# Kernel optimization log

Hardware: AMD Instinct MI355X
Metric: run time of the kernel (lower is better)

## Reference

```python
import jax, jax.numpy as jnp
import numpy as np

B, T, S, A = 4, 10, 6, 6
HID, L, IMG = 512, 6, 128
NCH = 16  # spatial-softmax channels
_px, _py = np.meshgrid(np.linspace(-1.0, 1.0, IMG), np.linspace(-1.0, 1.0, IMG))
POSX = jnp.asarray(_px.reshape(-1), jnp.float32)
POSY = jnp.asarray(_py.reshape(-1), jnp.float32)


def _conv_relu(x, w, b):
    y = jax.lax.conv_general_dilated(x, w, (1, 1), 'SAME',
                                     dimension_numbers=('NCHW', 'OIHW', 'NCHW'))
    return jax.nn.relu(y + b[None, :, None, None])


def _cnn_ss(x, ws, bs):
    for w, b in zip(ws, bs):
        x = _conv_relu(x, w, b)
    n = x.shape[0]
    attn = jax.nn.softmax(x.reshape(n, NCH, -1), axis=-1)  # (n, 16, H*W)
    ex = attn @ POSX  # (n, 16)
    ey = attn @ POSY
    return jnp.stack([ex, ey], axis=-1).reshape(n, 2 * NCH)  # (n, 32)


def _lstm_cell(x, h, c, wih, whh, bih, bhh):
    g = x @ wih.T + bih + h @ whh.T + bhh
    i, f, gg, o = jnp.split(g, 4, axis=-1)  # torch LSTMCell gate order i,f,g,o
    c2 = jax.nn.sigmoid(f) * c + jax.nn.sigmoid(i) * jnp.tanh(gg)
    h2 = jax.nn.sigmoid(o) * jnp.tanh(c2)
    return h2, c2


def setup_inputs() -> dict:
    key = jax.random.key(0)
    ks = iter(jax.random.split(key, 64))

    def nrm(shape, s=0.05):
        return jax.random.normal(next(ks), shape, dtype=jnp.float32) * s

    inp = {
        'seq_img_main': nrm((B, T, 3, IMG, IMG), 1.0),
        'seq_img_secondary': nrm((B, T, 3, IMG, IMG), 1.0),
        'seq_states': nrm((B, T, S), 1.0),
    }
    chans = [(32, 3), (64, 32), (128, 64), (16, 128)]
    for cam in ('m', 's'):
        for j, (o, ci) in enumerate(chans):
            inp[f'{cam}_w{j}'] = nrm((o, ci, 3, 3))
            inp[f'{cam}_b{j}'] = nrm((o,))
    in0, inr = S + 64, HID + 64  # 70 and 576
    inp['wih0'] = nrm((4 * HID, in0)); inp['whh0'] = nrm((4 * HID, HID))
    inp['bih0'] = nrm((4 * HID,)); inp['bhh0'] = nrm((4 * HID,))
    inp['wih_r'] = nrm((L - 1, 4 * HID, inr)); inp['whh_r'] = nrm((L - 1, 4 * HID, HID))
    inp['bih_r'] = nrm((L - 1, 4 * HID)); inp['bhh_r'] = nrm((L - 1, 4 * HID))
    inp['out_w'] = nrm((A, inr)); inp['out_b'] = nrm((A,))
    return inp


def reference(seq_img_main, seq_img_secondary, seq_states,
              m_w0, m_b0, m_w1, m_b1, m_w2, m_b2, m_w3, m_b3,
              s_w0, s_b0, s_w1, s_b1, s_w2, s_b2, s_w3, s_b3,
              wih0, whh0, bih0, bhh0, wih_r, whh_r, bih_r, bhh_r,
              out_w, out_b):
    b, t = seq_img_main.shape[:2]
    fm = _cnn_ss(seq_img_main.reshape(b * t, 3, IMG, IMG),
                 [m_w0, m_w1, m_w2, m_w3], [m_b0, m_b1, m_b2, m_b3])
    fs = _cnn_ss(seq_img_secondary.reshape(b * t, 3, IMG, IMG),
                 [s_w0, s_w1, s_w2, s_w3], [s_b0, s_b1, s_b2, s_b3])
    img = jnp.concatenate([fm, fs], axis=-1).reshape(b, t, 64)  # (B,T,64)

    h0 = jnp.zeros((L, b, HID), jnp.float32)
    c0 = jnp.zeros((L, b, HID), jnp.float32)

    def step(carry, xt):
        h, c = carry
        st, im = xt  # (B,S), (B,64)
        x = jnp.concatenate([st, im], axis=-1)
        hn, cn = _lstm_cell(x, h[0], c[0], wih0, whh0, bih0, bhh0)
        hs, cs = [hn], [cn]
        for l in range(L - 1):
            x = jnp.concatenate([hs[-1], im], axis=-1)
            hl, cl = _lstm_cell(x, h[l + 1], c[l + 1],
                                wih_r[l], whh_r[l], bih_r[l], bhh_r[l])
            hs.append(hl); cs.append(cl)
        out = jnp.concatenate([hs[-1], im], axis=-1) @ out_w.T + out_b
        return (jnp.stack(hs), jnp.stack(cs)), out

    _, outs = jax.lax.scan(step, (h0, c0),
                           (seq_states.transpose(1, 0, 2), img.transpose(1, 0, 2)))
    return outs.transpose(1, 0, 2)  # (B,T,A)
```

## Files before the change

kernel.cpp:

```cpp
#include <hip/hip_runtime.h>
#include <hip/hip_bf16.h>
#include <math.h>

typedef __hip_bfloat16 bf16;
typedef short bf16x8 __attribute__((ext_vector_type(8)));
typedef float f32x4 __attribute__((ext_vector_type(4)));

static constexpr int HWPX = 16384;
static constexpr int NBL  = 16;

__device__ inline float sigmoidf_(float x) { return 1.0f / (1.0f + expf(-x)); }
__device__ inline float bflo(unsigned u) { return __uint_as_float(u << 16); }
__device__ inline float bfhi(unsigned u) { return __uint_as_float(u & 0xffff0000u); }
__device__ inline int swz(int x) { return (x ^ (x >> 2)) & 3; }

__device__ inline void gll16(const bf16* g, short* l) {
    __builtin_amdgcn_global_load_lds(
        (const __attribute__((address_space(1))) void*)g,
        (__attribute__((address_space(3))) void*)l, 16, 0, 0);
}

__global__ __launch_bounds__(256) void prep_lstm_k(
    const float* __restrict__ wih0, const float* __restrict__ whh0,
    const float* __restrict__ wihr, const float* __restrict__ whhr,
    bf16* __restrict__ d0, bf16* __restrict__ d1,
    bf16* __restrict__ d2, bf16* __restrict__ d3)
{
    const size_t nA = 2048ull * 72, nB = 2048ull * 512;
    const size_t nC = 5ull * 2048 * 576, nD = 5ull * 2048 * 512;
    for (size_t i = blockIdx.x * 256ull + threadIdx.x; i < nA + nB + nC + nD;
         i += (size_t)gridDim.x * 256) {
        if (i < nA) {
            int c = (int)(i % 72), r = (int)(i / 72);
            d0[i] = __float2bfloat16(c < 70 ? wih0[(size_t)r * 70 + c] : 0.f);
        } else if (i < nA + nB) {
            size_t k = i - nA; d1[k] = __float2bfloat16(whh0[k]);
        } else if (i < nA + nB + nC) {
            size_t k = i - nA - nB; d2[k] = __float2bfloat16(wihr[k]);
        } else {
            size_t k = i - nA - nB - nC; d3[k] = __float2bfloat16(whhr[k]);
        }
    }
}

struct ConvW {
    const float* src[8];
    bf16* dst[8];
};

__global__ __launch_bounds__(256) void prep_conv_k(ConvW a)
{
    const int sizes[4] = {3072, 18432, 73728, 18432};
    const int cins[4] = {3, 32, 64, 128};
    const int couts[4] = {32, 64, 128, 16};
    int total = 2 * 113664;
    for (int idx = blockIdx.x * 256 + threadIdx.x; idx < total; idx += gridDim.x * 256) {
        int i = idx, cam = 0;
        if (i >= 113664) { cam = 1; i -= 113664; }
        int layer = 0;
        while (layer < 3 && i >= sizes[layer]) { i -= sizes[layer]; ++layer; }
        const float* w = a.src[cam * 4 + layer];
        bf16* d = a.dst[cam * 4 + layer];
        if (layer == 0) {
            int k = i & 31, co = (i >> 5) & 31, ky = i >> 10;
            int kx = k >> 3, c = k & 7;
            float v = (kx < 3 && c < 3) ? w[((co * 3 + c) * 3 + ky) * 3 + kx] : 0.f;
            d[i] = __float2bfloat16(v);
        } else {
            int CIN = cins[layer], COUT = couts[layer], KC = CIN / 32;
            int e = i & 7;
            int t2 = i >> 3;
            int co = t2 % COUT;
            int t3 = t2 / COUT;
            int q = t3 & 3;
            int t4 = t3 >> 2;
            int kc = t4 % KC;
            int tap = t4 / KC;
            d[i] = __float2bfloat16(w[((size_t)(co * CIN + kc * 32 + q * 8 + e)) * 9 + tap]);
        }
    }
}

__global__ __launch_bounds__(256) void conv0_nhwc(
    const float* __restrict__ srcm, const float* __restrict__ srcs,
    const bf16* __restrict__ w0m, const bf16* __restrict__ w0s,
    const float* __restrict__ bm, const float* __restrict__ bs,
    bf16* __restrict__ out, int c0)
{
    const int y = blockIdx.x;
    const int cam = blockIdx.y;
    const int img = blockIdx.z;
    const int ci_ = cam * gridDim.z + img;
    const float* inImg = (cam ? srcs : srcm) + (size_t)(c0 + img) * 3 * HWPX;
    const bf16* wT0 = cam ? w0s : w0m;
    const float* bias = cam ? bs : bm;
    const int tid = threadIdx.x;
    const int wave = tid >> 6, lane = tid & 63;
    const int wm = wave & 1, wn = wave >> 1;
    const int q = lane >> 4, n16 = lane & 15;

    __shared__ short smem[3 * 130 * 16];

    for (int d = tid; d < 3 * 130; d += 256) {
        int x = d % 130, r = d / 130;
        int yy = y + r - 1, xx = x - 1;
        bf16 v8[8];
#pragma unroll
        for (int c = 0; c < 8; ++c) v8[c] = __float2bfloat16(0.f);
        if ((unsigned)yy < 128u && (unsigned)xx < 128u) {
            int o = yy * 128 + xx;
            v8[0] = __float2bfloat16(inImg[o]);
            v8[1] = __float2bfloat16(inImg[HWPX + o]);
            v8[2] = __float2bfloat16(inImg[2 * HWPX + o]);
        }
        *(bf16x8*)(void*)&smem[(r * 130 + x) * 16] = *(bf16x8*)(void*)v8;
        *(bf16x8*)(void*)&smem[(r * 130 + x) * 16 + 8] = (bf16x8)0;
    }
    __syncthreads();

    f32x4 acc[4];
#pragma unroll
    for (int nt = 0; nt < 4; ++nt) acc[nt] = f32x4{0.f, 0.f, 0.f, 0.f};

    const int co = wm * 16 + n16;
#pragma unroll
    for (int ky = 0; ky < 3; ++ky) {
        bf16x8 aF = *(const bf16x8*)(const void*)(wT0 + ((size_t)(ky * 32 + co) * 32) + q * 8);
#pragma unroll
        for (int nt = 0; nt < 4; ++nt) {
            int x = (wn * 4 + nt) * 16 + n16;
            int off = (q < 3) ? (ky * 130 + x + q) * 16 : (ky * 130 + x) * 16 + 8;
            bf16x8 bF = *(const bf16x8*)(const void*)&smem[off];
            acc[nt] = __builtin_amdgcn_mfma_f32_16x16x32_bf16(aF, bF, acc[nt], 0, 0, 0);
        }
    }

    int co0 = wm * 16 + q * 4;
#pragma unroll
    for (int nt = 0; nt < 4; ++nt) {
        int x = (wn * 4 + nt) * 16 + n16;
        bf16 tmp[4];
#pragma unroll
        for (int r = 0; r < 4; ++r) {
            float v = acc[nt][r] + bias[co0 + r];
            tmp[r] = __float2bfloat16(v > 0.f ? v : 0.f);
        }
        *reinterpret_cast<uint2*>(out + ((size_t)ci_ * HWPX + y * 128 + x) * 32 + co0)
            = *reinterpret_cast<uint2*>(tmp);
    }
}

template <int CIN, int COUT>
__global__ __launch_bounds__(256, 4) void conv2r(
    const bf16* __restrict__ in, const bf16* __restrict__ wTm,
    const bf16* __restrict__ wTs, const float* __restrict__ bm,
    const float* __restrict__ bs, bf16* __restrict__ out,
    const char* __restrict__ zpage)
{
    constexpr int KC = CIN / 32;
    constexpr int NB = (KC > 1) ? 2 : 1;
    constexpr int MW = COUT / 32;
    constexpr int SLOTS = 4 * 264;

    const int y0 = (blockIdx.x >> 1) * 2;
    const int x0 = (blockIdx.x & 1) * 64;
    const int cam = blockIdx.y;
    const int img = blockIdx.z;
    const int ci_ = cam * gridDim.z + img;
    const bf16* wT = cam ? wTs : wTm;
    const float* bias = cam ? bs : bm;
    const int tid = threadIdx.x;
    const int wave = tid >> 6, lane = tid & 63;
    const int wrow = wave >> 1, wm = wave & 1;
    const int q = lane >> 4, n16 = lane & 15;

    __shared__ short smem[NB][SLOTS * 8];
    const bf16* inImg = in + (size_t)ci_ * HWPX * CIN;

    const bf16* sptr[5];
#pragma unroll
    for (int it = 0; it < 5; ++it) {
        int s = it * 256 + tid;
        int r = s / 264, s2 = s - r * 264;
        int sx = s2 >> 2;
        int g = (s2 & 3) ^ swz(sx);
        int yy = y0 + r - 1, xx = x0 + sx - 1;
        bool ok = (s < SLOTS) && ((unsigned)yy < 128u) && ((unsigned)xx < 128u);
        sptr[it] = ok ? inImg + ((size_t)yy * 128 + xx) * CIN + g * 8
                      : (const bf16*)(zpage + (tid & 255) * 16);
    }
    auto stage = [&](int kc, int buf) {
#pragma unroll
        for (int it = 0; it < 5; ++it) {
            if (it * 256 + tid < SLOTS)
                gll16(sptr[it] + kc * 32, &smem[buf][it * 2048 + wave * 512]);
        }
    };

    f32x4 acc[MW][4];
#pragma unroll
    for (int mt = 0; mt < MW; ++mt)
#pragma unroll
        for (int nt = 0; nt < 4; ++nt) acc[mt][nt] = f32x4{0.f, 0.f, 0.f, 0.f};

    stage(0, 0);
    for (int kc = 0; kc < KC; ++kc) {
        __syncthreads();
        if (kc + 1 < KC) stage(kc + 1, (kc + 1) % NB);
        const short* sb = smem[kc % NB];
#pragma unroll
        for (int ky = 0; ky < 3; ++ky) {
#pragma unroll
            for (int kx = 0; kx < 3; ++kx) {
                bf16x8 aF[MW];
#pragma unroll
                for (int mt = 0; mt < MW; ++mt) {
                    int co = (wm * MW + mt) * 16 + n16;
                    aF[mt] = *(const bf16x8*)(const void*)(wT +
                        ((((size_t)(ky * 3 + kx) * KC + kc) * 4 + q) * COUT + co) * 8);
                }
#pragma unroll
                for (int nt = 0; nt < 4; ++nt) {
                    int xt = nt * 16 + n16 + kx;
                    int slot = (wrow + ky) * 264 + xt * 4 + (q ^ swz(xt));
                    bf16x8 bF = *(const bf16x8*)(const void*)&sb[slot * 8];
#pragma unroll
                    for (int mt = 0; mt < MW; ++mt)
                        acc[mt][nt] = __builtin_amdgcn_mfma_f32_16x16x32_bf16(
                            aF[mt], bF, acc[mt][nt], 0, 0, 0);
                }
            }
        }
    }

    const int y = y0 + wrow;
#pragma unroll
    for (int mt = 0; mt < MW; ++mt) {
        int co0 = (wm * MW + mt) * 16 + q * 4;
#pragma unroll
        for (int nt = 0; nt < 4; ++nt) {
            int x = x0 + nt * 16 + n16;
            bf16 tmp[4];
#pragma unroll
            for (int r = 0; r < 4; ++r) {
                float v = acc[mt][nt][r] + bias[co0 + r];
                tmp[r] = __float2bfloat16(v > 0.f ? v : 0.f);
            }
            *reinterpret_cast<uint2*>(out + ((size_t)ci_ * HWPX + y * 128 + x) * COUT + co0)
                = *reinterpret_cast<uint2*>(tmp);
        }
    }
}

__global__ __launch_bounds__(256, 6) void conv4_xs(
    const bf16* __restrict__ in, const bf16* __restrict__ wTm,
    const bf16* __restrict__ wTs, const float* __restrict__ bm,
    const float* __restrict__ bs,
    float* __restrict__ partial,
    const char* __restrict__ zpage, int c0)
{
    constexpr int CIN = 128, COUT = 16, KC = 4;
    constexpr int SLOTS = 3 * 66 * 4;
    const int y = blockIdx.x >> 1;
    const int xh = blockIdx.x & 1;
    const int x0 = xh * 64;
    const int cam = blockIdx.y;
    const int img = blockIdx.z;
    const int ci_ = cam * gridDim.z + img;
    const int gimg = cam * 40 + c0 + img;
    const bf16* wT = cam ? wTs : wTm;
    const float* bias = cam ? bs : bm;
    const int tid = threadIdx.x;
    const int wave = tid >> 6, lane = tid & 63;
    const int q = lane >> 4, n16 = lane & 15;

    __shared__ short smem[2][SLOTS * 8];
    __shared__ float sred[3][4][16];
    const bf16* inImg = in + (size_t)ci_ * HWPX * CIN;

    const bf16* sptr[4];
#pragma unroll
    for (int it = 0; it < 4; ++it) {
        int s = it * 256 + tid;
        int r = s / 264, s2 = s - r * 264;
        int sx = s2 >> 2;
        int g = (s2 & 3) ^ swz(sx);
        int yy = y + r - 1, xx = x0 + sx - 1;
        bool ok = (s < SLOTS) && ((unsigned)yy < 128u) && ((unsigned)xx < 128u);
        sptr[it] = ok ? inImg + ((size_t)yy * 128 + xx) * CIN + g * 8
                      : (const bf16*)(zpage + (tid & 255) * 16);
    }
    auto stage = [&](int kc, int buf) {
#pragma unroll
        for (int it = 0; it < 4; ++it) {
            if (it * 256 + tid < SLOTS)
                gll16(sptr[it] + kc * 32, &smem[buf][it * 2048 + wave * 512]);
        }
    };

    f32x4 acc = f32x4{0.f, 0.f, 0.f, 0.f};

    stage(0, 0);
    for (int kc = 0; kc < KC; ++kc) {
        __syncthreads();
        if (kc + 1 < KC) stage(kc + 1, (kc + 1) & 1);
        const short* sb = smem[kc & 1];
#pragma unroll
        for (int ky = 0; ky < 3; ++ky) {
#pragma unroll
            for (int kx = 0; kx < 3; ++kx) {
                bf16x8 aF = *(const bf16x8*)(const void*)(wT +
                    ((((size_t)(ky * 3 + kx) * KC + kc) * 4 + q) * COUT + n16) * 8);
                int xt = wave * 16 + n16 + kx;
                int slot = xt * 4 + (q ^ swz(xt));
                bf16x8 bF = *(const bf16x8*)(const void*)&sb[ky * 2112 + slot * 8];
                acc = __builtin_amdgcn_mfma_f32_16x16x32_bf16(aF, bF, acc, 0, 0, 0);
            }
        }
    }

    float v[4];
    int x = x0 + wave * 16 + n16;
    float px = -1.f + (2.f / 127.f) * x;
#pragma unroll
    for (int r = 0; r < 4; ++r) {
        float t = acc[r] + bias[q * 4 + r];
        v[r] = t > 0.f ? t : 0.f;
    }
    float M[4];
#pragma unroll
    for (int r = 0; r < 4; ++r) {
        M[r] = v[r];
        M[r] = fmaxf(M[r], __shfl_xor(M[r], 1));
        M[r] = fmaxf(M[r], __shfl_xor(M[r], 2));
        M[r] = fmaxf(M[r], __shfl_xor(M[r], 4));
        M[r] = fmaxf(M[r], __shfl_xor(M[r], 8));
    }
    if (n16 == 0)
#pragma unroll
        for (int r = 0; r < 4; ++r) sred[0][wave][q * 4 + r] = M[r];
    __syncthreads();
#pragma unroll
    for (int r = 0; r < 4; ++r) {
        M[r] = fmaxf(fmaxf(sred[0][0][q * 4 + r], sred[0][1][q * 4 + r]),
                     fmaxf(sred[0][2][q * 4 + r], sred[0][3][q * 4 + r]));
    }
    float s[4], sx[4];
#pragma unroll
    for (int r = 0; r < 4; ++r) {
        float e = expf(v[r] - M[r]);
        s[r] = e; sx[r] = e * px;
        s[r] += __shfl_xor(s[r], 1);  sx[r] += __shfl_xor(sx[r], 1);
        s[r] += __shfl_xor(s[r], 2);  sx[r] += __shfl_xor(sx[r], 2);
        s[r] += __shfl_xor(s[r], 4);  sx[r] += __shfl_xor(sx[r], 4);
        s[r] += __shfl_xor(s[r], 8);  sx[r] += __shfl_xor(sx[r], 8);
    }
    __syncthreads();
    if (n16 == 0)
#pragma unroll
        for (int r = 0; r < 4; ++r) {
            sred[1][wave][q * 4 + r] = s[r];
            sred[2][wave][q * 4 + r] = sx[r];
        }
    __syncthreads();
    if (tid < 16) {
        float S = sred[1][0][tid] + sred[1][1][tid] + sred[1][2][tid] + sred[1][3][tid];
        float SX = sred[2][0][tid] + sred[2][1][tid] + sred[2][2][tid] + sred[2][3][tid];
        float Mv = fmaxf(fmaxf(sred[0][0][tid], sred[0][1][tid]),
                         fmaxf(sred[0][2][tid], sred[0][3][tid]));
        float* pp = partial + (((size_t)gimg * 16 + tid) * 256 + (y * 2 + xh)) * 4;
        pp[0] = Mv; pp[1] = S; pp[2] = SX;
    }
}

__global__ __launch_bounds__(256) void ssmerge_k(
    const float* __restrict__ partial, float* __restrict__ featm,
    float* __restrict__ feats)
{
    const int img = blockIdx.x;
    const int cam = img / 40, li = img % 40;
    float* feat = cam ? feats : featm;
    const int tid = threadIdx.x;
    const int co = tid >> 4, s = tid & 15;
    const float* base = partial + ((size_t)img * 16 + co) * 256 * 4;
    float M = -1e30f, S = 0.f, SX = 0.f, SY = 0.f;
    for (int i = s; i < 256; i += 16) {
        float m = base[i * 4], sv = base[i * 4 + 1], sxv = base[i * 4 + 2];
        float py = -1.f + (2.f / 127.f) * (i >> 1);
        float Mn = fmaxf(M, m);
        float w0 = expf(M - Mn), w1 = expf(m - Mn);
        S = S * w0 + sv * w1;
        SX = SX * w0 + sxv * w1;
        SY = SY * w0 + sv * py * w1;
        M = Mn;
    }
#pragma unroll
    for (int mask = 1; mask < 16; mask <<= 1) {
        float Mo = __shfl_xor(M, mask), So = __shfl_xor(S, mask);
        float SXo = __shfl_xor(SX, mask), SYo = __shfl_xor(SY, mask);
        float Mn = fmaxf(M, Mo);
        float w0 = expf(M - Mn), w1 = expf(Mo - Mn);
        S = S * w0 + So * w1; SX = SX * w0 + SXo * w1; SY = SY * w0 + SYo * w1;
        M = Mn;
    }
    if (s == 0) {
        feat[(size_t)li * 32 + 2 * co] = SX / S;
        feat[(size_t)li * 32 + 2 * co + 1] = SY / S;
    }
}

__device__ inline float imgfeat(const float* featm, const float* feats,
                                int b, int t, int k)
{
    int idx = (b * 10 + t) * 32;
    return k < 32 ? featm[idx + k] : feats[idx + k - 32];
}

template <int NB1>
__device__ inline void cell_mm(const bf16* __restrict__ wih,
                               const bf16* __restrict__ whh,
                               const float* __restrict__ xs0,
                               int j, int sub, float (&dg)[4][4])
{
    constexpr int K1 = NB1 * 8;
    constexpr int XS = K1 + 512;
#pragma unroll
    for (int r = 0; r < 4; ++r) {
        const uint4* __restrict__ w1 =
            reinterpret_cast<const uint4*>(wih + (size_t)(j + r * 512) * K1);
#pragma unroll
        for (int g0 = 0; g0 < NB1; g0 += 8) {
            int g = g0 + sub;
            if (g0 + 7 < NB1 || g < NB1) {
                uint4 u = w1[g];
                float a0 = bflo(u.x), a1 = bfhi(u.x), a2 = bflo(u.y), a3 = bfhi(u.y);
                float a4 = bflo(u.z), a5 = bfhi(u.z), a6 = bflo(u.w), a7 = bfhi(u.w);
#pragma unroll
                for (int b = 0; b < 4; ++b) {
                    const float* xp = xs0 + b * XS + g * 8;
                    dg[r][b] += a0 * xp[0] + a1 * xp[1] + a2 * xp[2] + a3 * xp[3]
                              + a4 * xp[4] + a5 * xp[5] + a6 * xp[6] + a7 * xp[7];
                }
            }
        }
        const uint4* __restrict__ w2 =
            reinterpret_cast<const uint4*>(whh + (size_t)(j + r * 512) * 512);
#pragma unroll
        for (int gi = 0; gi < 8; ++gi) {
            int g = gi * 8 + sub;
            uint4 u = w2[g];
            float a0 = bflo(u.x), a1 = bfhi(u.x), a2 = bflo(u.y), a3 = bfhi(u.y);
            float a4 = bflo(u.z), a5 = bfhi(u.z), a6 = bflo(u.w), a7 = bfhi(u.w);
#pragma unroll
            for (int b = 0; b < 4; ++b) {
                const float* xp = xs0 + b * XS + K1 + g * 8;
                dg[r][b] += a0 * xp[0] + a1 * xp[1] + a2 * xp[2] + a3 * xp[3]
                          + a4 * xp[4] + a5 * xp[5] + a6 * xp[6] + a7 * xp[7];
            }
        }
    }
}

template <int NB1>
__device__ inline void cell_step(
    int l, int t, int bx,
    const bf16* __restrict__ wih, const bf16* __restrict__ whh,
    const float* __restrict__ bih, const float* __restrict__ bhh,
    const float* __restrict__ states,
    const float* __restrict__ featm, const float* __restrict__ feats,
    float* __restrict__ hAll, float* __restrict__ cst,
    float* __restrict__ xs)
{
    constexpr int K1 = NB1 * 8;
    constexpr int XS = K1 + 512;
    const int tid = threadIdx.x;
    const int jloc = tid >> 3;
    const int sub = tid & 7;
    const int j = bx * 32 + jloc;

    const float* hprev = (l == 0) ? nullptr
                       : hAll + ((size_t)(t + 1) * 6 + (l - 1)) * 2048;
    const float* hold  = hAll + ((size_t)t * 6 + l) * 2048;
    float* hnew        = hAll + ((size_t)(t + 1) * 6 + l) * 2048;

    if (NB1 == 72) {
        for (int i = tid; i < 4 * 512; i += 256) {
            int bb = i >> 9, kk = i & 511;
            float2 cv;
            int base;
            if (kk < 256) {
                cv = *reinterpret_cast<const float2*>(&hprev[bb * 512 + kk * 2]);
                base = bb * XS + kk * 2;
            } else {
                cv = *reinterpret_cast<const float2*>(&hold[bb * 512 + (kk - 256) * 2]);
                base = bb * XS + 576 + (kk - 256) * 2;
            }
            xs[base] = cv.x; xs[base + 1] = cv.y;
        }
        {
            int bb = tid >> 6, k = tid & 63;
            xs[bb * XS + 512 + k] = imgfeat(featm, feats, bb, t, k);
        }
    } else {
        for (int i = tid; i < 4 * 256; i += 256) {
            int bb = i >> 8, kk = i & 255;
            float2 cv = *reinterpret_cast<const float2*>(&hold[bb * 512 + kk * 2]);
            int base = bb * XS + 72 + kk * 2;
            xs[base] = cv.x; xs[base + 1] = cv.y;
        }
        for (int i = tid; i < 4 * 72; i += 256) {
            int bb = i / 72, k = i - bb * 72;
            float v = (k < 6) ? states[(bb * 10 + t) * 6 + k]
                              : (k < 70 ? imgfeat(featm, feats, bb, t, k - 6) : 0.f);
            xs[bb * XS + k] = v;
        }
    }
    __syncthreads();

    float dg[4][4] = {{0.f, 0.f, 0.f, 0.f}, {0.f, 0.f, 0.f, 0.f},
                      {0.f, 0.f, 0.f, 0.f}, {0.f, 0.f, 0.f, 0.f}};
    cell_mm<NB1>(wih, whh, xs, j, sub, dg);

#pragma unroll
    for (int r = 0; r < 4; ++r)
#pragma unroll
        for (int b = 0; b < 4; ++b) {
            dg[r][b] += __shfl_xor(dg[r][b], 1);
            dg[r][b] += __shfl_xor(dg[r][b], 2);
            dg[r][b] += __shfl_xor(dg[r][b], 4);
        }

    if (sub == 0) {
        float b0 = bih[j] + bhh[j];
        float b1 = bih[j + 512] + bhh[j + 512];
        float b2 = bih[j + 1024] + bhh[j + 1024];
        float b3 = bih[j + 1536] + bhh[j + 1536];
#pragma unroll
        for (int b = 0; b < 4; ++b) {
            float gi = dg[0][b] + b0;
            float gf = dg[1][b] + b1;
            float gg = dg[2][b] + b2;
            float go = dg[3][b] + b3;
            float cp = cst[b * 512 + j];
            float c2 = sigmoidf_(gf) * cp + sigmoidf_(gi) * tanhf(gg);
            float h2 = sigmoidf_(go) * tanhf(c2);
            cst[b * 512 + j] = c2;
            hnew[b * 512 + j] = h2;
        }
    }
}

__global__ __launch_bounds__(256) void lstm_diag2_k(
    const bf16* __restrict__ wih0p, const bf16* __restrict__ whh0b,
    const bf16* __restrict__ wihrb, const bf16* __restrict__ whhrb,
    const float* __restrict__ bih0, const float* __restrict__ bhh0,
    const float* __restrict__ bihr, const float* __restrict__ bhhr,
    const float* __restrict__ states,
    const float* __restrict__ featm, const float* __restrict__ feats,
    float* __restrict__ hAll, float* __restrict__ cAll,
    const float* __restrict__ out_w, const float* __restrict__ out_b,
    float* __restrict__ out, int d)
{
    const int l = blockIdx.y;
    const int bx = blockIdx.x;
    const int tid = threadIdx.x;
    __shared__ float xs[4 * 1088];

    if (l == 6) {
        int t = d - 6;
        if (t < 0 || t >= 10 || bx != 0) return;
        const float* h5 = hAll + ((size_t)(t + 1) * 6 + 5) * 2048;
        int p = tid >> 3, sub = tid & 7;
        if (p >= 24) return;
        int b = p / 6, a = p % 6;
        const float* wr = out_w + a * 576;
        float acc = 0.f;
        for (int k = sub; k < 256; k += 8) {
            float2 cv = *reinterpret_cast<const float2*>(&h5[b * 512 + k * 2]);
            acc += wr[k * 2] * cv.x + wr[k * 2 + 1] * cv.y;
        }
        for (int k = sub; k < 64; k += 8)
            acc += wr[512 + k] * imgfeat(featm, feats, b, t, k);
        acc += __shfl_xor(acc, 1);
        acc += __shfl_xor(acc, 2);
        acc += __shfl_xor(acc, 4);
        if (sub == 0) out[(b * 10 + t) * 6 + a] = acc + out_b[a];
        return;
    }

    const int t = d - l;
    if (t < 0 || t >= 10) return;

    float* cst = cAll + (size_t)l * 2048;
    if (l == 0) {
        cell_step<9>(0, t, bx, wih0p, whh0b, bih0, bhh0,
                     states, featm, feats, hAll, cst, xs);
    } else {
        const bf16* wih = wihrb + (size_t)(l - 1) * 2048 * 576;
        const bf16* whh = whhrb + (size_t)(l - 1) * 2048 * 512;
        const float* bih = bihr + (l - 1) * 2048;
        const float* bhh = bhhr + (l - 1) * 2048;
        cell_step<72>(l, t, bx, wih, whh, bih, bhh,
                      states, featm, feats, hAll, cst, xs);
    }
}

extern "C" void kernel_launch(void* const* d_in, const int* in_sizes, int n_in,
                              void* d_out, int out_size, void* d_ws, size_t ws_size,
                              hipStream_t stream)
{
    const float* seq_m = (const float*)d_in[0];
    const float* seq_s = (const float*)d_in[1];
    const float* states = (const float*)d_in[2];
    const float *cw[2][4], *cb[2][4];
    for (int cam = 0; cam < 2; ++cam)
        for (int j = 0; j < 4; ++j) {
            cw[cam][j] = (const float*)d_in[3 + cam * 8 + j * 2];
            cb[cam][j] = (const float*)d_in[3 + cam * 8 + j * 2 + 1];
        }
    const float* wih0  = (const float*)d_in[19];
    const float* whh0  = (const float*)d_in[20];
    const float* bih0  = (const float*)d_in[21];
    const float* bhh0  = (const float*)d_in[22];
    const float* wih_r = (const float*)d_in[23];
    const float* whh_r = (const float*)d_in[24];
    const float* bih_r = (const float*)d_in[25];
    const float* bhh_r = (const float*)d_in[26];
    const float* out_w = (const float*)d_in[27];
    const float* out_b = (const float*)d_in[28];
    float* out = (float*)d_out;

    char* wsc = (char*)d_ws;
    auto carve = [&](size_t bytes) {
        char* p = wsc;
        wsc += (bytes + 255) & ~(size_t)255;
        return p;
    };
    float* featm = (float*)carve(40 * 32 * 4);
    float* feats = (float*)carve(40 * 32 * 4);
    float* hAll  = (float*)carve((size_t)11 * 6 * 2048 * 4);
    float* cAll  = (float*)carve((size_t)6 * 2048 * 4);
    char*  zpage = carve(8192);
    float* partial = (float*)carve((size_t)80 * 16 * 256 * 4 * 4);
    const int wtElts[4] = {3072, 18432, 73728, 18432};
    bf16* wT[2][4];
    for (int cam = 0; cam < 2; ++cam)
        for (int j = 0; j < 4; ++j) wT[cam][j] = (bf16*)carve(wtElts[j] * 2);
    bf16* wih0p = (bf16*)carve((size_t)2048 * 72 * 2);
    bf16* whh0b = (bf16*)carve((size_t)2048 * 512 * 2);
    bf16* wihrb = (bf16*)carve((size_t)5 * 2048 * 576 * 2);
    bf16* whhrb = (bf16*)carve((size_t)5 * 2048 * 512 * 2);

    size_t used = (size_t)(wsc - (char*)d_ws);
    size_t rem = ws_size > used ? ws_size - used : 0;
    int CHI = 1;
    const int cands[7] = {20, 10, 8, 5, 4, 2, 1};
    for (int i = 0; i < 7; ++i) {
        size_t need = (size_t)2 * cands[i] * (128 + 64) * HWPX * 2;
        if (need <= rem) { CHI = cands[i]; break; }
    }
    bf16* bufA = (bf16*)carve((size_t)2 * CHI * HWPX * 128 * 2);
    bf16* bufB = (bf16*)carve((size_t)2 * CHI * HWPX * 64 * 2);

    hipMemsetAsync(hAll, 0, 6 * 2048 * 4, stream);
    hipMemsetAsync(cAll, 0, 6 * 2048 * 4, stream);
    hipMemsetAsync(zpage, 0, 8192, stream);

    prep_lstm_k<<<2048, 256, 0, stream>>>(wih0, whh0, wih_r, whh_r,
                                          wih0p, whh0b, wihrb, whhrb);
    ConvW cwArg;
    for (int cam = 0; cam < 2; ++cam)
        for (int j = 0; j < 4; ++j) {
            cwArg.src[cam * 4 + j] = cw[cam][j];
            cwArg.dst[cam * 4 + j] = wT[cam][j];
        }
    prep_conv_k<<<888, 256, 0, stream>>>(cwArg);

    for (int c0 = 0; c0 < 40; c0 += CHI) {
        int ch = (40 - c0) < CHI ? (40 - c0) : CHI;
        conv0_nhwc<<<dim3(128, 2, ch), 256, 0, stream>>>(
            seq_m, seq_s, wT[0][0], wT[1][0], cb[0][0], cb[1][0], bufA, c0);
        conv2r<32, 64><<<dim3(128, 2, ch), 256, 0, stream>>>(
            bufA, wT[0][1], wT[1][1], cb[0][1], cb[1][1], bufB, zpage);
        conv2r<64, 128><<<dim3(128, 2, ch), 256, 0, stream>>>(
            bufB, wT[0][2], wT[1][2], cb[0][2], cb[1][2], bufA, zpage);
        conv4_xs<<<dim3(256, 2, ch), 256, 0, stream>>>(
            bufA, wT[0][3], wT[1][3], cb[0][3], cb[1][3], partial, zpage, c0);
    }
    ssmerge_k<<<80, 256, 0, stream>>>(partial, featm, feats);

    for (int d = 0; d < 16; ++d) {
        lstm_diag2_k<<<dim3(16, 7), 256, 0, stream>>>(
            wih0p, whh0b, wihrb, whhrb, bih0, bhh0, bih_r, bhh_r,
            states, featm, feats, hAll, cAll, out_w, out_b, out, d);
    }
}
```

Measured before the change: 1.149 ms.

## Fuse first two conv layers into one kernel with halo recompute in LDS

Merges conv0 (3->32) and conv1 (32->64) into a single kernel. Each block recomputes the conv0 output for a 2-row by 64-column tile plus a halo and stores it in swizzled LDS, then runs conv1 straight from LDS. This removes the global write and read of the 32-channel intermediate and one kernel launch, at the cost of redundant halo compute and more LDS per block. It also adds a chunk-size candidate of 40 images so that all images can be processed in one pass when the workspace allows.

```diff
diff --git a/kernel.cpp b/kernel.cpp
--- a/kernel.cpp
+++ b/kernel.cpp
@@ -7,7 +7,6 @@
 typedef float f32x4 __attribute__((ext_vector_type(4)));
 
 static constexpr int HWPX = 16384;
-static constexpr int NBL  = 16;
 
 __device__ inline float sigmoidf_(float x) { return 1.0f / (1.0f + expf(-x)); }
 __device__ inline float bflo(unsigned u) { return __uint_as_float(u << 16); }
@@ -81,29 +80,41 @@
     }
 }
 
-__global__ __launch_bounds__(256) void conv0_nhwc(
+__global__ __launch_bounds__(256, 4) void conv01(
     const float* __restrict__ srcm, const float* __restrict__ srcs,
     const bf16* __restrict__ w0m, const bf16* __restrict__ w0s,
+    const float* __restrict__ b0m, const float* __restrict__ b0s,
+    const bf16* __restrict__ wTm, const bf16* __restrict__ wTs,
     const float* __restrict__ bm, const float* __restrict__ bs,
     bf16* __restrict__ out, int c0)
 {
-    const int y = blockIdx.x;
+    constexpr int COUT = 64, MW = 2;
+    constexpr int SLOTS = 4 * 264;
+
+    const int y0 = (blockIdx.x >> 1) * 2;
+    const int x0 = (blockIdx.x & 1) * 64;
     const int cam = blockIdx.y;
     const int img = blockIdx.z;
     const int ci_ = cam * gridDim.z + img;
     const float* inImg = (cam ? srcs : srcm) + (size_t)(c0 + img) * 3 * HWPX;
     const bf16* wT0 = cam ? w0s : w0m;
+    const float* bias0 = cam ? b0s : b0m;
+    const bf16* wT = cam ? wTs : wTm;
     const float* bias = cam ? bs : bm;
     const int tid = threadIdx.x;
     const int wave = tid >> 6, lane = tid & 63;
-    const int wm = wave & 1, wn = wave >> 1;
+    const int wrow = wave >> 1, wm = wave & 1;
     const int q = lane >> 4, n16 = lane & 15;
 
-    __shared__ short smem[3 * 130 * 16];
-
-    for (int d = tid; d < 3 * 130; d += 256) {
-        int x = d % 130, r = d / 130;
-        int yy = y + r - 1, xx = x - 1;
+    __shared__ short smem[SLOTS * 8];
+    __shared__ short raw[6 * 68 * 16];
+
+    for (int i = tid; i < SLOTS; i += 256)
+        *(bf16x8*)(void*)&smem[i * 8] = (bf16x8)0;
+
+    for (int d = tid; d < 6 * 68; d += 256) {
+        int x = d % 68, r = d / 68;
+        int yy = y0 - 2 + r, xx = x0 - 2 + x;
         bf16 v8[8];
 #pragma unroll
         for (int c = 0; c < 8; ++c) v8[c] = __float2bfloat16(0.f);
@@ -113,40 +124,91 @@
             v8[1] = __float2bfloat16(inImg[HWPX + o]);
             v8[2] = __float2bfloat16(inImg[2 * HWPX + o]);
         }
-        *(bf16x8*)(void*)&smem[(r * 130 + x) * 16] = *(bf16x8*)(void*)v8;
-        *(bf16x8*)(void*)&smem[(r * 130 + x) * 16 + 8] = (bf16x8)0;
+        *(bf16x8*)(void*)&raw[d * 16] = *(bf16x8*)(void*)v8;
+        *(bf16x8*)(void*)&raw[d * 16 + 8] = (bf16x8)0;
     }
     __syncthreads();
 
-    f32x4 acc[4];
-#pragma unroll
-    for (int nt = 0; nt < 4; ++nt) acc[nt] = f32x4{0.f, 0.f, 0.f, 0.f};
-
-    const int co = wm * 16 + n16;
+    const int co0_ = wm * 16 + n16;
+    for (int rp = 0; rp < 4; ++rp) {
+        int Y = y0 - 1 + rp;
+        if ((unsigned)Y >= 128u) continue;
+        for (int xg = wrow; xg < 5; xg += 2) {
+            int xt = xg * 16 + n16;
+            int xts = xt < 66 ? xt : 65;
+            f32x4 a0 = f32x4{0.f, 0.f, 0.f, 0.f};
+#pragma unroll
+            for (int ky = 0; ky < 3; ++ky) {
+                bf16x8 aF = *(const bf16x8*)(const void*)(wT0 +
+                    ((size_t)(ky * 32 + co0_) * 32) + q * 8);
+                int off = (q < 3) ? ((rp + ky) * 68 + xts + q) * 16
+                                  : ((rp + ky) * 68 + xts) * 16 + 8;
+                bf16x8 bF = *(const bf16x8*)(const void*)&raw[off];
+                a0 = __builtin_amdgcn_mfma_f32_16x16x32_bf16(aF, bF, a0, 0, 0, 0);
+            }
+            int X = x0 - 1 + xt;
+            if (xt < 66 && (unsigned)X < 128u) {
+                int cb0 = wm * 16 + q * 4;
+                bf16 tmp[4];
+#pragma unroll
+                for (int r = 0; r < 4; ++r) {
+                    float v = a0[r] + bias0[cb0 + r];
+                    tmp[r] = __float2bfloat16(v > 0.f ? v : 0.f);
+                }
+                int g = cb0 >> 3;
+                int sbase = (rp * 264 + xt * 4 + (g ^ swz(xt))) * 8 + (q & 1) * 4;
+                *reinterpret_cast<uint2*>(&smem[sbase]) = *reinterpret_cast<uint2*>(tmp);
+            }
+        }
+    }
+    __syncthreads();
+
+    f32x4 acc[MW][4];
+#pragma unroll
+    for (int mt = 0; mt < MW; ++mt)
+#pragma unroll
+        for (int nt = 0; nt < 4; ++nt) acc[mt][nt] = f32x4{0.f, 0.f, 0.f, 0.f};
+
 #pragma unroll
     for (int ky = 0; ky < 3; ++ky) {
-        bf16x8 aF = *(const bf16x8*)(const void*)(wT0 + ((size_t)(ky * 32 + co) * 32) + q * 8);
+#pragma unroll
+        for (int kx = 0; kx < 3; ++kx) {
+            bf16x8 aF[MW];
+#pragma unroll
+            for (int mt = 0; mt < MW; ++mt) {
+                int co = (wm * MW + mt) * 16 + n16;
+                aF[mt] = *(const bf16x8*)(const void*)(wT +
+                    (((size_t)(ky * 3 + kx) * 4 + q) * COUT + co) * 8);
+            }
+#pragma unroll
+            for (int nt = 0; nt < 4; ++nt) {
+                int xt = nt * 16 + n16 + kx;
+                int slot = (wrow + ky) * 264 + xt * 4 + (q ^ swz(xt));
+                bf16x8 bF = *(const bf16x8*)(const void*)&smem[slot * 8];
+#pragma unroll
+                for (int mt = 0; mt < MW; ++mt)
+                    acc[mt][nt] = __builtin_amdgcn_mfma_f32_16x16x32_bf16(
+                        aF[mt], bF, acc[mt][nt], 0, 0, 0);
+            }
+        }
+    }
+
+    const int y = y0 + wrow;
+#pragma unroll
+    for (int mt = 0; mt < MW; ++mt) {
+        int co0 = (wm * MW + mt) * 16 + q * 4;
 #pragma unroll
         for (int nt = 0; nt < 4; ++nt) {
-            int x = (wn * 4 + nt) * 16 + n16;
-            int off = (q < 3) ? (ky * 130 + x + q) * 16 : (ky * 130 + x) * 16 + 8;
-            bf16x8 bF = *(const bf16x8*)(const void*)&smem[off];
-            acc[nt] = __builtin_amdgcn_mfma_f32_16x16x32_bf16(aF, bF, acc[nt], 0, 0, 0);
-        }
-    }
-
-    int co0 = wm * 16 + q * 4;
-#pragma unroll
-    for (int nt = 0; nt < 4; ++nt) {
-        int x = (wn * 4 + nt) * 16 + n16;
-        bf16 tmp[4];
-#pragma unroll
-        for (int r = 0; r < 4; ++r) {
-            float v = acc[nt][r] + bias[co0 + r];
-            tmp[r] = __float2bfloat16(v > 0.f ? v : 0.f);
-        }
-        *reinterpret_cast<uint2*>(out + ((size_t)ci_ * HWPX + y * 128 + x) * 32 + co0)
-            = *reinterpret_cast<uint2*>(tmp);
+            int x = x0 + nt * 16 + n16;
+            bf16 tmp[4];
+#pragma unroll
+            for (int r = 0; r < 4; ++r) {
+                float v = acc[mt][nt][r] + bias[co0 + r];
+                tmp[r] = __float2bfloat16(v > 0.f ? v : 0.f);
+            }
+            *reinterpret_cast<uint2*>(out + ((size_t)ci_ * HWPX + y * 128 + x) * COUT + co0)
+                = *reinterpret_cast<uint2*>(tmp);
+        }
     }
 }
 
@@ -654,8 +716,8 @@
     size_t used = (size_t)(wsc - (char*)d_ws);
     size_t rem = ws_size > used ? ws_size - used : 0;
     int CHI = 1;
-    const int cands[7] = {20, 10, 8, 5, 4, 2, 1};
-    for (int i = 0; i < 7; ++i) {
+    const int cands[8] = {40, 20, 10, 8, 5, 4, 2, 1};
+    for (int i = 0; i < 8; ++i) {
         size_t need = (size_t)2 * cands[i] * (128 + 64) * HWPX * 2;
         if (need <= rem) { CHI = cands[i]; break; }
     }
@@ -678,10 +740,9 @@
 
     for (int c0 = 0; c0 < 40; c0 += CHI) {
         int ch = (40 - c0) < CHI ? (40 - c0) : CHI;
-        conv0_nhwc<<<dim3(128, 2, ch), 256, 0, stream>>>(
-            seq_m, seq_s, wT[0][0], wT[1][0], cb[0][0], cb[1][0], bufA, c0);
-        conv2r<32, 64><<<dim3(128, 2, ch), 256, 0, stream>>>(
-            bufA, wT[0][1], wT[1][1], cb[0][1], cb[1][1], bufB, zpage);
+        conv01<<<dim3(128, 2, ch), 256, 0, stream>>>(
+            seq_m, seq_s, wT[0][0], wT[1][0], cb[0][0], cb[1][0],
+            wT[0][1], wT[1][1], cb[0][1], cb[1][1], bufB, c0);
         conv2r<64, 128><<<dim3(128, 2, ch), 256, 0, stream>>>(
             bufB, wT[0][2], wT[1][2], cb[0][2], cb[1][2], bufA, zpage);
         conv4_xs<<<dim3(256, 2, ch), 256, 0, stream>>>(
```

Result: no change. 1.132 ms (-1.6%).
